# Kernel optimization log

Hardware: AMD Instinct MI355X
Metric: run time of the kernel (lower is better)

Reference implementation:

```python
import jax, jax.numpy as jnp
import numpy as np

# Model config (mirrors Mamba2Block(dim=256) with mamba_ssm defaults)
D_MODEL = 256
EXPAND = 2
D_INNER = D_MODEL * EXPAND          # 512
HEADDIM = D_MODEL * EXPAND // 8     # 64
NHEADS = D_INNER // HEADDIM         # 8
D_STATE = 64
D_CONV = 4
CONV_DIM = D_INNER + 2 * D_STATE    # 640 (ngroups=1)
D_IN_PROJ = 2 * D_INNER + 2 * D_STATE + NHEADS  # 1160
BATCH, SEQLEN = 2, 2048
EPS = 1e-5


def setup_inputs() -> dict:
    key = jax.random.key(0)
    ks = jax.random.split(key, 12)
    s = 0.02
    return {
        "hidden_states": jax.random.normal(ks[0], (BATCH, SEQLEN, D_MODEL), jnp.float32),
        "norm_w": jnp.ones((D_MODEL,), jnp.float32),
        "norm_b": jnp.zeros((D_MODEL,), jnp.float32),
        "W_in": jax.random.normal(ks[1], (D_MODEL, D_IN_PROJ), jnp.float32) * s,
        "conv_w": jax.random.normal(ks[2], (CONV_DIM, D_CONV), jnp.float32) * 0.25,
        "conv_b": jnp.zeros((CONV_DIM,), jnp.float32),
        "dt_bias": jax.random.uniform(ks[3], (NHEADS,), jnp.float32),
        "A_log": jax.random.uniform(ks[4], (NHEADS,), jnp.float32),  # A = -exp(A_log) in (-e, -1]
        "D_param": jnp.ones((NHEADS,), jnp.float32),
        "rms_w": jnp.ones((D_INNER,), jnp.float32),
        "W_out": jax.random.normal(ks[5], (D_INNER, D_MODEL), jnp.float32) * s,
    }


def _layer_norm(x, w, b):
    mu = jnp.mean(x, -1, keepdims=True)
    var = jnp.mean((x - mu) ** 2, -1, keepdims=True)
    return (x - mu) * jax.lax.rsqrt(var + EPS) * w + b


def _causal_depthwise_conv(x, w, b):
    # x: [B,L,C], w: [C,K] depthwise causal conv
    B, L, C = x.shape
    K = w.shape[1]
    xp = jnp.pad(x, ((0, 0), (K - 1, 0), (0, 0)))
    y = b
    for k in range(K):  # K=4, fixed small kernel
        y = y + w[:, k] * xp[:, k:k + L, :]
    return y


def reference(hidden_states, norm_w, norm_b, W_in, conv_w, conv_b, dt_bias, A_log, D_param, rms_w, W_out):
    B, L, D = hidden_states.shape
    residual = hidden_states                       # residual is None, drop_path=0
    x = _layer_norm(residual, norm_w, norm_b)      # pre-norm

    zxbcdt = jnp.einsum("bld,de->ble", x, W_in)    # [B,L,2*Di+2*N+H]
    z = zxbcdt[..., :D_INNER]
    xBC = zxbcdt[..., D_INNER:D_INNER + CONV_DIM]
    dt = zxbcdt[..., -NHEADS:]

    xBC = jax.nn.silu(_causal_depthwise_conv(xBC, conv_w, conv_b))
    xs = xBC[..., :D_INNER]
    Bm = xBC[..., D_INNER:D_INNER + D_STATE]       # [B,L,N] (ngroups=1)
    Cm = xBC[..., D_INNER + D_STATE:]              # [B,L,N]

    dt = jax.nn.softplus(dt + dt_bias)             # [B,L,H]
    A = -jnp.exp(A_log)                            # [H]
    dA = jnp.exp(dt * A)                           # [B,L,H]

    xh = xs.reshape(B, L, NHEADS, HEADDIM)         # [B,L,H,P]
    dtx = dt[..., None] * xh                       # [B,L,H,P]

    def step(s, inp):
        dA_t, dtx_t, B_t, C_t = inp                # [B,H],[B,H,P],[B,N],[B,N]
        s = s * dA_t[:, :, None, None] + dtx_t[..., None] * B_t[:, None, None, :]
        y_t = jnp.einsum("bhpn,bn->bhp", s, C_t)
        return s, y_t

    s0 = jnp.zeros((B, NHEADS, HEADDIM, D_STATE), hidden_states.dtype)
    xs_in = (jnp.swapaxes(dA, 0, 1), jnp.swapaxes(dtx, 0, 1),
             jnp.swapaxes(Bm, 0, 1), jnp.swapaxes(Cm, 0, 1))
    _, ys = jax.lax.scan(step, s0, xs_in)          # ys: [L,B,H,P]
    y = jnp.swapaxes(ys, 0, 1) + D_param[None, None, :, None] * xh  # skip term
    y = y.reshape(B, L, D_INNER)

    # gated RMSNorm (norm_before_gate=False): rmsnorm(y * silu(z)) * rms_w
    g = y * jax.nn.silu(z)
    g = g * jax.lax.rsqrt(jnp.mean(g * g, -1, keepdims=True) + EPS) * rms_w

    out = jnp.einsum("bld,de->ble", g, W_out)
    return out, residual
```

## Files before the change

kernel.cpp:

```cpp
#include <hip/hip_runtime.h>
#include <hip/hip_bf16.h>

#define BATCH 2
#define SEQLEN 2048
#define DMODEL 256
#define DINNER 512
#define NHEADS 8
#define HEADDIM 64
#define DSTATE 64
#define CONVDIM 640
#define DINPROJ 1160
#define NTOK (BATCH*SEQLEN)
#define Q 64
#define NCH (SEQLEN/Q)
#define NPAD_IN 1216
#define TS 72
#define RS2 198

typedef short v8s __attribute__((ext_vector_type(8)));
typedef float v4f __attribute__((ext_vector_type(4)));

__device__ __forceinline__ unsigned short f2bf(float f){
    __hip_bfloat16 h = __float2bfloat16(f);
    return *reinterpret_cast<unsigned short*>(&h);
}
__device__ __forceinline__ float bf2f(unsigned short u){
    unsigned int x = ((unsigned int)u) << 16;
    return __uint_as_float(x);
}

__global__ __launch_bounds__(256) void k_ln(
        const float* __restrict__ hid, const float* __restrict__ nw, const float* __restrict__ nb,
        float* __restrict__ res, unsigned short* __restrict__ Xb){
    __shared__ float xs[16][DMODEL];
    int t = threadIdx.x, tok0 = blockIdx.x*16;
    for(int i=0;i<16;i++){
        int idx = i*256+t; int j = idx>>8, c = idx&255;
        float v = hid[(size_t)(tok0+j)*DMODEL + c];
        xs[j][c] = v;
        res[(size_t)(tok0+j)*DMODEL + c] = v;
    }
    __syncthreads();
    int g = t>>4, il = t&15;
    float sum=0.f, sumsq=0.f;
    for(int i=0;i<16;i++){ float v = xs[g][il*16+i]; sum += v; sumsq += v*v; }
    #pragma unroll
    for(int m=1;m<16;m<<=1){ sum += __shfl_xor(sum,m); sumsq += __shfl_xor(sumsq,m); }
    float mu   = sum*(1.f/256.f);
    float var  = sumsq*(1.f/256.f) - mu*mu;
    float rstd = rsqrtf(var + 1e-5f);
    for(int i=0;i<16;i++){
        int c = il*16+i;
        xs[g][c] = (xs[g][c]-mu)*rstd*nw[c] + nb[c];
    }
    __syncthreads();
    for(int i=0;i<16;i++){
        int idx = i*256+t; int j = idx>>8, c = idx&255;
        Xb[(size_t)(tok0+j)*DMODEL + c] = f2bf(xs[j][c]);
    }
}

__global__ __launch_bounds__(256) void k_cvt(const float* __restrict__ Win, const float* __restrict__ Wout,
                                             unsigned short* __restrict__ Wti, unsigned short* __restrict__ Wto){
    int bx = blockIdx.x;
    if(bx < NPAD_IN/4){
        int n0 = bx*4, k = threadIdx.x;
        #pragma unroll
        for(int i=0;i<4;i++){
            int n = n0+i;
            float v = (n < DINPROJ) ? Win[(size_t)k*DINPROJ + n] : 0.f;
            Wti[(size_t)n*DMODEL + k] = f2bf(v);
        }
    } else {
        int n0 = (bx - NPAD_IN/4)*4;
        #pragma unroll
        for(int kk=0;kk<2;kk++){
            int k = threadIdx.x + kk*256;
            #pragma unroll
            for(int i=0;i<4;i++){
                int n = n0+i;
                Wto[(size_t)n*DINNER + k] = f2bf(Wout[(size_t)k*DMODEL + n]);
            }
        }
    }
}

template<int BF16OUT>
__global__ __launch_bounds__(256) void k_gemm(
        const unsigned short* __restrict__ A, const unsigned short* __restrict__ Bt,
        float* __restrict__ Cf, unsigned short* __restrict__ Cb, int K, int Ncols){
    __shared__ __align__(16) unsigned short As[128*40];
    __shared__ __align__(16) unsigned short Bs[64*40];
    int t = threadIdx.x;
    int lane = t & 63, w = t >> 6;
    int lanelow = lane & 15, quad = lane >> 4;
    int tok0 = blockIdx.x * 128;
    int n0   = blockIdx.y * 64;
    v4f acc[2][4];
    #pragma unroll
    for(int mi=0;mi<2;mi++)
        #pragma unroll
        for(int ni=0;ni<4;ni++)
            acc[mi][ni] = (v4f){0.f,0.f,0.f,0.f};
    for(int k0=0; k0<K; k0+=32){
        __syncthreads();
        #pragma unroll
        for(int cc=0; cc<2; cc++){
            int c = t + cc*256;
            int row = c>>2, off = c&3;
            uint4 v = *(const uint4*)(A + (size_t)(tok0+row)*K + k0 + off*8);
            *(uint4*)&As[row*40 + off*8] = v;
        }
        {
            int row = t>>2, off = t&3;
            uint4 v = *(const uint4*)(Bt + (size_t)(n0+row)*K + k0 + off*8);
            *(uint4*)&Bs[row*40 + off*8] = v;
        }
        __syncthreads();
        v8s a0 = *(const v8s*)&As[(w*32 +      lanelow)*40 + quad*8];
        v8s a1 = *(const v8s*)&As[(w*32 + 16 + lanelow)*40 + quad*8];
        v8s b[4];
        #pragma unroll
        for(int ni=0;ni<4;ni++)
            b[ni] = *(const v8s*)&Bs[(ni*16 + lanelow)*40 + quad*8];
        #pragma unroll
        for(int ni=0;ni<4;ni++){
            acc[0][ni] = __builtin_amdgcn_mfma_f32_16x16x32_bf16(a0, b[ni], acc[0][ni], 0,0,0);
            acc[1][ni] = __builtin_amdgcn_mfma_f32_16x16x32_bf16(a1, b[ni], acc[1][ni], 0,0,0);
        }
    }
    #pragma unroll
    for(int mi=0;mi<2;mi++){
        #pragma unroll
        for(int ni=0;ni<4;ni++){
            int col = n0 + ni*16 + lanelow;
            if(col < Ncols){
                #pragma unroll
                for(int r=0;r<4;r++){
                    int row = tok0 + w*32 + mi*16 + quad*4 + r;
                    if(BF16OUT) Cb[(size_t)row*Ncols + col] = f2bf(acc[mi][ni][r]);
                    else        Cf[(size_t)row*Ncols + col] = acc[mi][ni][r];
                }
            }
        }
    }
}

__global__ __launch_bounds__(256) void k_chunk1(
        const unsigned short* __restrict__ zxb, const float* __restrict__ conv_w, const float* __restrict__ conv_b,
        const float* __restrict__ dt_bias, const float* __restrict__ A_log, const float* __restrict__ D_param,
        unsigned short* __restrict__ yw16, float* __restrict__ contrib,
        float* __restrict__ Larr, float* __restrict__ decayArr, unsigned short* __restrict__ Ccv){
    int blk = blockIdx.x;
    int c = blk & 31, h = (blk>>5)&7, b = blk>>8;
    int t = threadIdx.x;
    int lane = t & 63, w = t >> 6;
    int lanelow = lane & 15, quad = lane >> 4;
    __shared__ __align__(16) unsigned short raw[67*RS2];
    __shared__ __align__(16) unsigned short Cb[64*TS];
    __shared__ __align__(16) unsigned short Bb[64*TS];
    __shared__ __align__(16) unsigned short BtW[64*TS];
    __shared__ __align__(16) unsigned short Xt[64*TS];
    __shared__ float Ls[Q], dts[Q], wch[Q];
    unsigned short* Gbuf = raw;
    int l0 = c*Q;
    int bh = b*NHEADS + h;
    const unsigned short* zbase = zxb + (size_t)(b*SEQLEN + l0)*DINPROJ;
    for(int i=0;i<7;i++){
        int gidx = t + 256*i;
        if(gidx < 67*24){
            int row = gidx/24, g = gidx%24;
            int ltok = l0 - 3 + row;
            int gcol = (g<8) ? (DINNER + h*HEADDIM + g*8) : (2*DINNER + (g-8)*8);
            uint4 v;
            if(ltok >= 0) v = *(const uint4*)(zbase + (ptrdiff_t)(row-3)*DINPROJ + gcol);
            else { v.x=0; v.y=0; v.z=0; v.w=0; }
            int ch = (g<8) ? g*8 : 64 + (g-8)*8;
            unsigned int* d = (unsigned int*)&raw[row*RS2 + ch];
            d[0]=v.x; d[1]=v.y; d[2]=v.z; d[3]=v.w;
        }
    }
    if(t < Q){
        float v = bf2f(zbase[(size_t)t*DINPROJ + (DINPROJ-NHEADS) + h]) + dt_bias[h];
        float dt = (v > 20.f) ? v : log1pf(__expf(v));
        float A  = -__expf(A_log[h]);
        float ld = dt*A;
        #pragma unroll
        for(int off=1; off<64; off<<=1){
            float u = __shfl_up(ld, off);
            if(lane >= off) ld += u;
        }
        Ls[t] = ld; dts[t] = dt;
    }
    __syncthreads();
    float L63 = Ls[Q-1];
    if(t < Q) wch[t] = __expf(L63 - Ls[t]) * dts[t];
    __syncthreads();
    unsigned short* CcP = Ccv + ((size_t)b*NCH + c)*4096;
    for(int i=0;i<12;i++){
        int u = t + 256*i;
        int st = u & 63, c4 = u >> 6, ch = c4*4;
        float xk[4][4];
        #pragma unroll
        for(int k=0;k<4;k++){
            const unsigned short* rp = &raw[(st+k)*RS2 + ch];
            ushort2 p0 = *(const ushort2*)rp;
            ushort2 p1 = *(const ushort2*)(rp+2);
            xk[k][0]=bf2f(p0.x); xk[k][1]=bf2f(p0.y); xk[k][2]=bf2f(p1.x); xk[k][3]=bf2f(p1.y);
        }
        float wst = wch[st];
        #pragma unroll
        for(int j=0;j<4;j++){
            int chj = ch+j;
            int cc = (chj<64) ? (h*HEADDIM + chj) : (448 + chj);
            float4 wv = *(const float4*)&conv_w[cc*4];
            float acc = conv_b[cc] + wv.x*xk[0][j] + wv.y*xk[1][j] + wv.z*xk[2][j] + wv.w*xk[3][j];
            float sv = acc/(1.f+__expf(-acc));
            if(chj < 64){
                Xt[chj*TS + st] = f2bf(sv);
            } else if(chj < 128){
                int n = chj-64;
                Bb[st*TS + n]  = f2bf(sv);
                BtW[n*TS + st] = f2bf(sv*wst);
            } else {
                int n = chj-128;
                unsigned short sb = f2bf(sv);
                Cb[st*TS + n] = sb;
                if(h==0) CcP[st*64 + n] = sb;
            }
        }
    }
    __syncthreads();
    v4f g[4];
    #pragma unroll
    for(int nt=0;nt<4;nt++) g[nt] = (v4f){0.f,0.f,0.f,0.f};
    #pragma unroll
    for(int kk=0;kk<2;kk++){
        v8s a = *(const v8s*)&Cb[(w*16+lanelow)*TS + kk*32 + quad*8];
        #pragma unroll
        for(int nt=0;nt<4;nt++){
            v8s bb = *(const v8s*)&Bb[(nt*16+lanelow)*TS + kk*32 + quad*8];
            g[nt] = __builtin_amdgcn_mfma_f32_16x16x32_bf16(a, bb, g[nt], 0,0,0);
        }
    }
    float Lrow[4];
    #pragma unroll
    for(int r=0;r<4;r++) Lrow[r] = Ls[w*16 + quad*4 + r];
    #pragma unroll
    for(int nt=0;nt<4;nt++){
        int col = nt*16 + lanelow;
        float Lc = Ls[col], dtc = dts[col];
        #pragma unroll
        for(int r=0;r<4;r++){
            int rowg = w*16 + quad*4 + r;
            float val = (col <= rowg) ? g[nt][r] * __expf(Lrow[r]-Lc) * dtc : 0.f;
            Gbuf[rowg*TS + col] = f2bf(val);
        }
    }
    __syncthreads();
    v4f ya[4], sa[4];
    #pragma unroll
    for(int nt=0;nt<4;nt++){ ya[nt]=(v4f){0.f,0.f,0.f,0.f}; sa[nt]=(v4f){0.f,0.f,0.f,0.f}; }
    #pragma unroll
    for(int kk=0;kk<2;kk++){
        v8s ag = *(const v8s*)&Gbuf[(w*16+lanelow)*TS + kk*32 + quad*8];
        v8s ax = *(const v8s*)&Xt[(w*16+lanelow)*TS + kk*32 + quad*8];
        #pragma unroll
        for(int nt=0;nt<4;nt++){
            v8s bx = *(const v8s*)&Xt[(nt*16+lanelow)*TS + kk*32 + quad*8];
            v8s bw = *(const v8s*)&BtW[(nt*16+lanelow)*TS + kk*32 + quad*8];
            ya[nt] = __builtin_amdgcn_mfma_f32_16x16x32_bf16(ag, bx, ya[nt], 0,0,0);
            sa[nt] = __builtin_amdgcn_mfma_f32_16x16x32_bf16(ax, bw, sa[nt], 0,0,0);
        }
    }
    float Dp = D_param[h];
    #pragma unroll
    for(int nt=0;nt<4;nt++){
        int col = nt*16 + lanelow;
        #pragma unroll
        for(int r=0;r<4;r++){
            int i = w*16 + quad*4 + r;
            float xval = bf2f(Xt[col*TS + i]);
            yw16[((size_t)b*SEQLEN + l0 + i)*DINNER + h*HEADDIM + col] = f2bf(ya[nt][r] + Dp*xval);
            contrib[(((size_t)bh*NCH + c)*64 + i)*64 + col] = sa[nt][r];
        }
    }
    if(t < Q) Larr[((size_t)bh*NCH + c)*Q + t] = Ls[t];
    if(t == 0) decayArr[bh*NCH + c] = __expf(L63);
}

__global__ __launch_bounds__(256) void k_chunk2(const float* __restrict__ contrib,
                                                const float* __restrict__ decayArr,
                                                unsigned short* __restrict__ Sb){
    int bh = blockIdx.x >> 4;
    int part = blockIdx.x & 15;
    int e = part*256 + threadIdx.x;
    const size_t base = (size_t)bh*NCH*4096 + e;
    float vals[NCH];
    #pragma unroll
    for(int c=0;c<NCH;c++) vals[c] = contrib[base + (size_t)c*4096];
    float s = 0.f;
    #pragma unroll
    for(int c=0;c<NCH;c++){
        Sb[base + (size_t)c*4096] = f2bf(s);
        s = fmaf(s, decayArr[bh*NCH + c], vals[c]);
    }
}

__global__ __launch_bounds__(512) void k_tail(
        const unsigned short* __restrict__ Ccv, const unsigned short* __restrict__ Sb,
        const float* __restrict__ Larr, const unsigned short* __restrict__ yw16,
        const unsigned short* __restrict__ zxb, const float* __restrict__ rms_w,
        unsigned short* __restrict__ Gb){
    int blk = blockIdx.x;
    int c = blk & 31, b = blk >> 5;
    int t = threadIdx.x;
    int h = t >> 6, lane = t & 63;
    int lanelow = lane & 15, quad = lane >> 4;
    int bh = b*NHEADS + h;
    __shared__ float wsum[8][64];
    __shared__ float rstdS[64];
    const unsigned short* Cp = Ccv + ((size_t)b*NCH + c)*4096;
    const unsigned short* Sp = Sb + ((size_t)bh*NCH + c)*4096;
    v8s a[4][2];
    #pragma unroll
    for(int rt=0;rt<4;rt++){
        a[rt][0] = *(const v8s*)(Cp + (rt*16+lanelow)*64 + quad*8);
        a[rt][1] = *(const v8s*)(Cp + (rt*16+lanelow)*64 + 32 + quad*8);
    }
    v8s s[4][2];
    #pragma unroll
    for(int nt=0;nt<4;nt++){
        s[nt][0] = *(const v8s*)(Sp + (nt*16+lanelow)*64 + quad*8);
        s[nt][1] = *(const v8s*)(Sp + (nt*16+lanelow)*64 + 32 + quad*8);
    }
    float g[4][4][4];
    float sq[4][4];
    const float* Lp = Larr + ((size_t)bh*NCH + c)*Q;
    #pragma unroll
    for(int rt=0;rt<4;rt++){
        float eL[4];
        #pragma unroll
        for(int r=0;r<4;r++) eL[r] = __expf(Lp[rt*16 + quad*4 + r]);
        #pragma unroll
        for(int nt=0;nt<4;nt++){
            v4f acc = (v4f){0.f,0.f,0.f,0.f};
            acc = __builtin_amdgcn_mfma_f32_16x16x32_bf16(a[rt][0], s[nt][0], acc, 0,0,0);
            acc = __builtin_amdgcn_mfma_f32_16x16x32_bf16(a[rt][1], s[nt][1], acc, 0,0,0);
            int col = h*HEADDIM + nt*16 + lanelow;
            #pragma unroll
            for(int r=0;r<4;r++){
                int i = rt*16 + quad*4 + r;
                size_t tok = (size_t)b*SEQLEN + c*Q + i;
                float yv = acc[r]*eL[r] + bf2f(yw16[tok*DINNER + col]);
                float z  = bf2f(zxb[tok*DINPROJ + col]);
                float gg = yv * (z/(1.f+__expf(-z)));
                g[rt][nt][r] = gg;
                sq[rt][r] = (nt==0 ? gg*gg : sq[rt][r] + gg*gg);
            }
        }
    }
    #pragma unroll
    for(int rt=0;rt<4;rt++)
        #pragma unroll
        for(int r=0;r<4;r++){
            float v = sq[rt][r];
            #pragma unroll
            for(int m=1;m<16;m<<=1) v += __shfl_xor(v, m);
            sq[rt][r] = v;
        }
    if(lanelow==0){
        #pragma unroll
        for(int rt=0;rt<4;rt++)
            #pragma unroll
            for(int r=0;r<4;r++)
                wsum[h][rt*16 + quad*4 + r] = sq[rt][r];
    }
    __syncthreads();
    if(t < 64){
        float tot = 0.f;
        #pragma unroll
        for(int hh=0;hh<8;hh++) tot += wsum[hh][t];
        rstdS[t] = rsqrtf(tot*(1.f/512.f) + 1e-5f);
    }
    __syncthreads();
    #pragma unroll
    for(int rt=0;rt<4;rt++){
        #pragma unroll
        for(int nt=0;nt<4;nt++){
            int col = h*HEADDIM + nt*16 + lanelow;
            float rw = rms_w[col];
            #pragma unroll
            for(int r=0;r<4;r++){
                int i = rt*16 + quad*4 + r;
                Gb[((size_t)b*SEQLEN + c*Q + i)*DINNER + col] = f2bf(g[rt][nt][r] * rstdS[i] * rw);
            }
        }
    }
}

extern "C" void kernel_launch(void* const* d_in, const int* in_sizes, int n_in,
                              void* d_out, int out_size, void* d_ws, size_t ws_size,
                              hipStream_t stream) {
    const float* hid     = (const float*)d_in[0];
    const float* norm_w  = (const float*)d_in[1];
    const float* norm_b  = (const float*)d_in[2];
    const float* Win     = (const float*)d_in[3];
    const float* conv_w  = (const float*)d_in[4];
    const float* conv_b  = (const float*)d_in[5];
    const float* dt_bias = (const float*)d_in[6];
    const float* A_log   = (const float*)d_in[7];
    const float* D_param = (const float*)d_in[8];
    const float* rms_w   = (const float*)d_in[9];
    const float* Wout    = (const float*)d_in[10];

    float* ws = (float*)d_ws;
    float* contrib = ws;
    float* Larr    = contrib + (size_t)16*NCH*4096;
    float* decayA  = Larr + (size_t)16*NCH*Q;
    unsigned short* zxb  = (unsigned short*)(decayA + 512);
    unsigned short* yw16 = zxb + (size_t)NTOK*DINPROJ;
    unsigned short* Sb   = yw16 + (size_t)NTOK*DINNER;
    unsigned short* Ccv  = Sb + (size_t)16*NCH*4096;
    unsigned short* Xb   = Ccv + (size_t)BATCH*NCH*4096;
    unsigned short* Gb   = Xb + (size_t)NTOK*DMODEL;
    unsigned short* Wti  = Gb + (size_t)NTOK*DINNER;
    unsigned short* Wto  = Wti + (size_t)NPAD_IN*DMODEL;

    float* out = (float*)d_out;
    float* res = out + (size_t)NTOK*DMODEL;

    k_ln<<<NTOK/16, 256, 0, stream>>>(hid, norm_w, norm_b, res, Xb);
    k_cvt<<<NPAD_IN/4 + DMODEL/4, 256, 0, stream>>>(Win, Wout, Wti, Wto);
    k_gemm<1><<<dim3(NTOK/128, NPAD_IN/64), 256, 0, stream>>>(Xb, Wti, nullptr, zxb, DMODEL, DINPROJ);
    k_chunk1<<<BATCH*NHEADS*NCH, 256, 0, stream>>>(zxb, conv_w, conv_b, dt_bias, A_log, D_param,
                                                   yw16, contrib, Larr, decayA, Ccv);
    k_chunk2<<<256, 256, 0, stream>>>(contrib, decayA, Sb);
    k_tail<<<BATCH*NCH, 512, 0, stream>>>(Ccv, Sb, Larr, yw16, zxb, rms_w, Gb);
    k_gemm<0><<<dim3(NTOK/128, DMODEL/64), 256, 0, stream>>>(Gb, Wto, out, nullptr, DINNER, DMODEL);
}
```

Measured before the change: 150.3 us.

## Fuse LayerNorm and weight conversion into the projection GEMMs

Removes the separate LayerNorm and weight-conversion kernels. The input GEMM now computes per-token mean and rstd itself, normalizes fp32 activations while staging them to bf16 in shared memory, and converts W_in to bf16 on the fly with a transposed shared store. The output GEMM likewise converts W_out on load. This saves two launches and the intermediate bf16 buffers, but each of the 19 column blocks recomputes LN statistics and reloads hidden states, and weight loads become scalar strided fp32 reads with conversion inside the K loop.

```diff
diff --git a/kernel.cpp b/kernel.cpp
--- a/kernel.cpp
+++ b/kernel.cpp
@@ -29,66 +29,109 @@
     return __uint_as_float(x);
 }
 
-__global__ __launch_bounds__(256) void k_ln(
+__global__ __launch_bounds__(256) void k_gemm_in(
         const float* __restrict__ hid, const float* __restrict__ nw, const float* __restrict__ nb,
-        float* __restrict__ res, unsigned short* __restrict__ Xb){
-    __shared__ float xs[16][DMODEL];
-    int t = threadIdx.x, tok0 = blockIdx.x*16;
-    for(int i=0;i<16;i++){
-        int idx = i*256+t; int j = idx>>8, c = idx&255;
-        float v = hid[(size_t)(tok0+j)*DMODEL + c];
-        xs[j][c] = v;
-        res[(size_t)(tok0+j)*DMODEL + c] = v;
-    }
-    __syncthreads();
-    int g = t>>4, il = t&15;
-    float sum=0.f, sumsq=0.f;
-    for(int i=0;i<16;i++){ float v = xs[g][il*16+i]; sum += v; sumsq += v*v; }
-    #pragma unroll
-    for(int m=1;m<16;m<<=1){ sum += __shfl_xor(sum,m); sumsq += __shfl_xor(sumsq,m); }
-    float mu   = sum*(1.f/256.f);
-    float var  = sumsq*(1.f/256.f) - mu*mu;
-    float rstd = rsqrtf(var + 1e-5f);
-    for(int i=0;i<16;i++){
-        int c = il*16+i;
-        xs[g][c] = (xs[g][c]-mu)*rstd*nw[c] + nb[c];
-    }
-    __syncthreads();
-    for(int i=0;i<16;i++){
-        int idx = i*256+t; int j = idx>>8, c = idx&255;
-        Xb[(size_t)(tok0+j)*DMODEL + c] = f2bf(xs[j][c]);
-    }
-}
-
-__global__ __launch_bounds__(256) void k_cvt(const float* __restrict__ Win, const float* __restrict__ Wout,
-                                             unsigned short* __restrict__ Wti, unsigned short* __restrict__ Wto){
-    int bx = blockIdx.x;
-    if(bx < NPAD_IN/4){
-        int n0 = bx*4, k = threadIdx.x;
-        #pragma unroll
-        for(int i=0;i<4;i++){
-            int n = n0+i;
-            float v = (n < DINPROJ) ? Win[(size_t)k*DINPROJ + n] : 0.f;
-            Wti[(size_t)n*DMODEL + k] = f2bf(v);
-        }
-    } else {
-        int n0 = (bx - NPAD_IN/4)*4;
-        #pragma unroll
-        for(int kk=0;kk<2;kk++){
-            int k = threadIdx.x + kk*256;
-            #pragma unroll
-            for(int i=0;i<4;i++){
-                int n = n0+i;
-                Wto[(size_t)n*DINNER + k] = f2bf(Wout[(size_t)k*DMODEL + n]);
+        const float* __restrict__ Win, float* __restrict__ res, unsigned short* __restrict__ zxb){
+    __shared__ __align__(16) unsigned short As[128*40];
+    __shared__ __align__(16) unsigned short Bs[64*40];
+    __shared__ float muS[128], rsS[128], nwS[256], nbS[256];
+    int t = threadIdx.x;
+    int lane = t & 63, w = t >> 6;
+    int lanelow = lane & 15, quad = lane >> 4;
+    int tok0 = blockIdx.x*128, n0 = blockIdx.y*64;
+    nwS[t] = nw[t]; nbS[t] = nb[t];
+    {
+        int j = t>>1, hf = t&1;
+        const float* hp = hid + (size_t)(tok0+j)*DMODEL + hf*128;
+        float sum=0.f, sq=0.f;
+        #pragma unroll
+        for(int i=0;i<32;i++){
+            float4 v = *(const float4*)(hp + i*4);
+            sum += v.x+v.y+v.z+v.w;
+            sq  += v.x*v.x+v.y*v.y+v.z*v.z+v.w*v.w;
+        }
+        sum += __shfl_xor(sum,1); sq += __shfl_xor(sq,1);
+        if(hf==0){
+            float mu = sum*(1.f/256.f);
+            float var = sq*(1.f/256.f) - mu*mu;
+            muS[j] = mu; rsS[j] = rsqrtf(var + 1e-5f);
+        }
+    }
+    if(blockIdx.y==0){
+        const float4* hv = (const float4*)hid + (size_t)tok0*64;
+        float4* rv = (float4*)res + (size_t)tok0*64;
+        for(int i=0;i<32;i++) rv[i*256+t] = hv[i*256+t];
+    }
+    v4f acc[2][4];
+    #pragma unroll
+    for(int mi=0;mi<2;mi++)
+        #pragma unroll
+        for(int ni=0;ni<4;ni++)
+            acc[mi][ni] = (v4f){0.f,0.f,0.f,0.f};
+    __syncthreads();
+    for(int k0=0; k0<DMODEL; k0+=32){
+        if(k0) __syncthreads();
+        #pragma unroll
+        for(int cc=0; cc<2; cc++){
+            int u = t + cc*256;
+            int row = u>>2, off = u&3;
+            const float* hp = hid + (size_t)(tok0+row)*DMODEL + k0 + off*8;
+            float4 v0 = *(const float4*)hp;
+            float4 v1 = *(const float4*)(hp+4);
+            float mu = muS[row], rs = rsS[row];
+            int cb = k0 + off*8;
+            ushort4 lo, hi;
+            lo.x = f2bf((v0.x-mu)*rs*nwS[cb+0] + nbS[cb+0]);
+            lo.y = f2bf((v0.y-mu)*rs*nwS[cb+1] + nbS[cb+1]);
+            lo.z = f2bf((v0.z-mu)*rs*nwS[cb+2] + nbS[cb+2]);
+            lo.w = f2bf((v0.w-mu)*rs*nwS[cb+3] + nbS[cb+3]);
+            hi.x = f2bf((v1.x-mu)*rs*nwS[cb+4] + nbS[cb+4]);
+            hi.y = f2bf((v1.y-mu)*rs*nwS[cb+5] + nbS[cb+5]);
+            hi.z = f2bf((v1.z-mu)*rs*nwS[cb+6] + nbS[cb+6]);
+            hi.w = f2bf((v1.w-mu)*rs*nwS[cb+7] + nbS[cb+7]);
+            *(ushort4*)&As[row*40 + off*8]     = lo;
+            *(ushort4*)&As[row*40 + off*8 + 4] = hi;
+        }
+        #pragma unroll
+        for(int i=0;i<8;i++){
+            int u = t + 256*i;
+            int nl = u & 63, kl = u >> 6;
+            int n = n0 + nl;
+            float v = (n < DINPROJ) ? Win[(size_t)(k0+kl)*DINPROJ + n] : 0.f;
+            Bs[nl*40 + kl] = f2bf(v);
+        }
+        __syncthreads();
+        v8s a0 = *(const v8s*)&As[(w*32 +      lanelow)*40 + quad*8];
+        v8s a1 = *(const v8s*)&As[(w*32 + 16 + lanelow)*40 + quad*8];
+        v8s b[4];
+        #pragma unroll
+        for(int ni=0;ni<4;ni++)
+            b[ni] = *(const v8s*)&Bs[(ni*16 + lanelow)*40 + quad*8];
+        #pragma unroll
+        for(int ni=0;ni<4;ni++){
+            acc[0][ni] = __builtin_amdgcn_mfma_f32_16x16x32_bf16(a0, b[ni], acc[0][ni], 0,0,0);
+            acc[1][ni] = __builtin_amdgcn_mfma_f32_16x16x32_bf16(a1, b[ni], acc[1][ni], 0,0,0);
+        }
+    }
+    #pragma unroll
+    for(int mi=0;mi<2;mi++){
+        #pragma unroll
+        for(int ni=0;ni<4;ni++){
+            int col = n0 + ni*16 + lanelow;
+            if(col < DINPROJ){
+                #pragma unroll
+                for(int r=0;r<4;r++){
+                    int row = tok0 + w*32 + mi*16 + quad*4 + r;
+                    zxb[(size_t)row*DINPROJ + col] = f2bf(acc[mi][ni][r]);
+                }
             }
         }
     }
 }
 
-template<int BF16OUT>
-__global__ __launch_bounds__(256) void k_gemm(
-        const unsigned short* __restrict__ A, const unsigned short* __restrict__ Bt,
-        float* __restrict__ Cf, unsigned short* __restrict__ Cb, int K, int Ncols){
+__global__ __launch_bounds__(256) void k_gemm_out(
+        const unsigned short* __restrict__ Gb, const float* __restrict__ Wout,
+        float* __restrict__ out){
     __shared__ __align__(16) unsigned short As[128*40];
     __shared__ __align__(16) unsigned short Bs[64*40];
     int t = threadIdx.x;
@@ -102,19 +145,20 @@
         #pragma unroll
         for(int ni=0;ni<4;ni++)
             acc[mi][ni] = (v4f){0.f,0.f,0.f,0.f};
-    for(int k0=0; k0<K; k0+=32){
+    for(int k0=0; k0<DINNER; k0+=32){
         __syncthreads();
         #pragma unroll
         for(int cc=0; cc<2; cc++){
-            int c = t + cc*256;
-            int row = c>>2, off = c&3;
-            uint4 v = *(const uint4*)(A + (size_t)(tok0+row)*K + k0 + off*8);
+            int u = t + cc*256;
+            int row = u>>2, off = u&3;
+            uint4 v = *(const uint4*)(Gb + (size_t)(tok0+row)*DINNER + k0 + off*8);
             *(uint4*)&As[row*40 + off*8] = v;
         }
-        {
-            int row = t>>2, off = t&3;
-            uint4 v = *(const uint4*)(Bt + (size_t)(n0+row)*K + k0 + off*8);
-            *(uint4*)&Bs[row*40 + off*8] = v;
+        #pragma unroll
+        for(int i=0;i<8;i++){
+            int u = t + 256*i;
+            int nl = u & 63, kl = u >> 6;
+            Bs[nl*40 + kl] = f2bf(Wout[(size_t)(k0+kl)*DMODEL + n0 + nl]);
         }
         __syncthreads();
         v8s a0 = *(const v8s*)&As[(w*32 +      lanelow)*40 + quad*8];
@@ -134,13 +178,10 @@
         #pragma unroll
         for(int ni=0;ni<4;ni++){
             int col = n0 + ni*16 + lanelow;
-            if(col < Ncols){
-                #pragma unroll
-                for(int r=0;r<4;r++){
-                    int row = tok0 + w*32 + mi*16 + quad*4 + r;
-                    if(BF16OUT) Cb[(size_t)row*Ncols + col] = f2bf(acc[mi][ni][r]);
-                    else        Cf[(size_t)row*Ncols + col] = acc[mi][ni][r];
-                }
+            #pragma unroll
+            for(int r=0;r<4;r++){
+                int row = tok0 + w*32 + mi*16 + quad*4 + r;
+                out[(size_t)row*DMODEL + col] = acc[mi][ni][r];
             }
         }
     }
@@ -422,20 +463,15 @@
     unsigned short* yw16 = zxb + (size_t)NTOK*DINPROJ;
     unsigned short* Sb   = yw16 + (size_t)NTOK*DINNER;
     unsigned short* Ccv  = Sb + (size_t)16*NCH*4096;
-    unsigned short* Xb   = Ccv + (size_t)BATCH*NCH*4096;
-    unsigned short* Gb   = Xb + (size_t)NTOK*DMODEL;
-    unsigned short* Wti  = Gb + (size_t)NTOK*DINNER;
-    unsigned short* Wto  = Wti + (size_t)NPAD_IN*DMODEL;
+    unsigned short* Gb   = Ccv + (size_t)BATCH*NCH*4096;
 
     float* out = (float*)d_out;
     float* res = out + (size_t)NTOK*DMODEL;
 
-    k_ln<<<NTOK/16, 256, 0, stream>>>(hid, norm_w, norm_b, res, Xb);
-    k_cvt<<<NPAD_IN/4 + DMODEL/4, 256, 0, stream>>>(Win, Wout, Wti, Wto);
-    k_gemm<1><<<dim3(NTOK/128, NPAD_IN/64), 256, 0, stream>>>(Xb, Wti, nullptr, zxb, DMODEL, DINPROJ);
+    k_gemm_in<<<dim3(NTOK/128, NPAD_IN/64), 256, 0, stream>>>(hid, norm_w, norm_b, Win, res, zxb);
     k_chunk1<<<BATCH*NHEADS*NCH, 256, 0, stream>>>(zxb, conv_w, conv_b, dt_bias, A_log, D_param,
                                                    yw16, contrib, Larr, decayA, Ccv);
     k_chunk2<<<256, 256, 0, stream>>>(contrib, decayA, Sb);
     k_tail<<<BATCH*NCH, 512, 0, stream>>>(Ccv, Sb, Larr, yw16, zxb, rms_w, Gb);
-    k_gemm<0><<<dim3(NTOK/128, DMODEL/64), 256, 0, stream>>>(Gb, Wto, out, nullptr, DINNER, DMODEL);
-}
+    k_gemm_out<<<dim3(NTOK/128, DMODEL/64), 256, 0, stream>>>(Gb, Wout, out);
+}
```

New measurement: 165.6 us. +10.1%, slower.
